# Optimization experiments

Measured on AMD Instinct MI355X. Metric: run time of the kernel, lower is better.

The kernel has to match this reference:

```python
import jax, jax.numpy as jnp
import numpy as np

B, S, D, H = 4, 2048, 768, 12
DH = D // H          # 64 head dim
DF = 4 * D           # 3072 FFN hidden
EPS = 1e-5


def setup_inputs() -> dict:
    key = jax.random.key(0)
    ks = jax.random.split(key, 16)
    s = 0.02
    inp = {
        "Q": jax.random.normal(ks[0], (B, S, D), jnp.float32),
        "K": jax.random.normal(ks[1], (B, S, D), jnp.float32),
        "V": jax.random.normal(ks[2], (B, S, D), jnp.float32),
        "Wq": s * jax.random.normal(ks[3], (D, D), jnp.float32),
        "bq": jnp.zeros((D,), jnp.float32),
        "Wk": s * jax.random.normal(ks[4], (D, D), jnp.float32),
        "bk": jnp.zeros((D,), jnp.float32),
        "Wv": s * jax.random.normal(ks[5], (D, D), jnp.float32),
        "bv": jnp.zeros((D,), jnp.float32),
        "Wo": s * jax.random.normal(ks[6], (D, D), jnp.float32),
        "bo": jnp.zeros((D,), jnp.float32),
        "ln_g": jnp.ones((D,), jnp.float32),
        "ln_b": jnp.zeros((D,), jnp.float32),
        "W1": s * jax.random.normal(ks[7], (D, DF), jnp.float32),
        "b1": jnp.zeros((DF,), jnp.float32),
        "W2": s * jax.random.normal(ks[8], (DF, D), jnp.float32),
        "b2": jnp.zeros((D,), jnp.float32),
    }
    return inp


def _split_heads(x):  # [B,S,D] -> [B,H,S,DH]
    return x.reshape(B, S, H, DH).transpose(0, 2, 1, 3)


def _layernorm(x, g, b):
    mu = jnp.mean(x, axis=-1, keepdims=True)
    var = jnp.mean(jnp.square(x - mu), axis=-1, keepdims=True)
    return (x - mu) * jax.lax.rsqrt(var + EPS) * g + b


def reference(Q, K, V, Wq, bq, Wk, bk, Wv, bv, Wo, bo, ln_g, ln_b, W1, b1, W2, b2):
    q = _split_heads(Q @ Wq + bq)            # [B,H,S,DH]
    k = _split_heads(K @ Wk + bk)
    v = _split_heads(V @ Wv + bv)
    scale = 1.0 / jnp.sqrt(jnp.asarray(DH, q.dtype))
    scores = jnp.einsum("bhqd,bhkd->bhqk", q, k) * scale   # [B,H,S,S]
    attn = jax.nn.softmax(scores, axis=-1)
    ctx = jnp.einsum("bhqk,bhkd->bhqd", attn, v)            # [B,H,S,DH]
    ctx = ctx.transpose(0, 2, 1, 3).reshape(B, S, D)
    attn_out = ctx @ Wo + bo
    h = _layernorm(Q + attn_out, ln_g, ln_b)                # residual + LN
    ff = jax.nn.gelu(h @ W1 + b1, approximate=False) @ W2 + b2
    return ff
```

## Files before the change

### kernel.cpp

```cpp
#include <hip/hip_runtime.h>
#include <hip/hip_bf16.h>
#include <math.h>

#define Bsz 4
#define Ssz 2048
#define Dsz 768
#define Hn  12
#define DHn 64
#define DFn 3072
#define NTOK (Bsz*Ssz)
#define EPSL 1e-5f

typedef __attribute__((ext_vector_type(8))) short bf16x8;
typedef __attribute__((ext_vector_type(4))) float f32x4;

__device__ __forceinline__ unsigned short f2bf(float f) {
    unsigned int u = __float_as_uint(f);
    u += 0x7fffu + ((u >> 16) & 1u);
    return (unsigned short)(u >> 16);
}
__device__ __forceinline__ float bf2f(unsigned short h) {
    return __uint_as_float(((unsigned int)h) << 16);
}

#define GLDS(gp, lp) __builtin_amdgcn_global_load_lds( \
    (const __attribute__((address_space(1))) void*)(gp), \
    (__attribute__((address_space(3))) void*)(lp), 16, 0, 0)

__device__ __forceinline__ void swizzle_mn(int bid, int mtot, int nb, int& m, int& n)
{
    const int xcd = bid & 7;
    const int idx = bid >> 3;
    m = xcd * (mtot >> 3) + idx / nb;
    n = idx % nb;
}

__global__ __launch_bounds__(256)
void wsplit_k(const float* __restrict__ W, unsigned short* __restrict__ Wh,
              unsigned short* __restrict__ Wl, int K, int N)
{
    __shared__ float tile[32][33];
    const int n0 = blockIdx.x * 32, k0 = blockIdx.y * 32;
    const int x = threadIdx.x, y = threadIdx.y;
    #pragma unroll
    for (int i = 0; i < 4; i++)
        tile[y + 8 * i][x] = W[(size_t)(k0 + y + 8 * i) * N + n0 + x];
    __syncthreads();
    #pragma unroll
    for (int i = 0; i < 4; i++) {
        float v = tile[x][y + 8 * i];
        unsigned short hb = f2bf(v);
        size_t o = (size_t)(n0 + y + 8 * i) * K + k0 + x;
        Wh[o] = hb;
        Wl[o] = f2bf(v - bf2f(hb));
    }
}

__global__ __launch_bounds__(256)
void presplit_k(const float* __restrict__ Qf, const float* __restrict__ Kf,
                const float* __restrict__ Vf,
                unsigned short* __restrict__ Qh, unsigned short* __restrict__ Ql,
                unsigned short* __restrict__ Kh, unsigned short* __restrict__ Kl,
                unsigned short* __restrict__ Vh)
{
    const int blocksPerSeg = (NTOK * Dsz) / 2048;
    const int seg = blockIdx.x / blocksPerSeg;
    const int idx = ((blockIdx.x % blocksPerSeg) * 256 + threadIdx.x) * 8;
    const float* src = (seg == 0) ? Qf : (seg == 1) ? Kf : Vf;

    float4 a = *(const float4*)(src + idx);
    float4 b = *(const float4*)(src + idx + 4);
    float fv[8] = {a.x, a.y, a.z, a.w, b.x, b.y, b.z, b.w};

    bf16x8 h8, l8;
    #pragma unroll
    for (int e = 0; e < 8; e++) {
        unsigned short hb = f2bf(fv[e]);
        h8[e] = (short)hb;
        l8[e] = (short)f2bf(fv[e] - bf2f(hb));
    }
    unsigned short* Hp = (seg == 0) ? Qh : (seg == 1) ? Kh : Vh;
    *(bf16x8*)(Hp + idx) = h8;
    if (seg < 2) {
        unsigned short* Lp = (seg == 0) ? Ql : Kl;
        *(bf16x8*)(Lp + idx) = l8;
    }
}

__global__ __launch_bounds__(256)
void qkv_mfma(const unsigned short* __restrict__ Qsh, const unsigned short* __restrict__ Qsl,
              const unsigned short* __restrict__ Ksh, const unsigned short* __restrict__ Ksl,
              const unsigned short* __restrict__ Vsh,
              const unsigned short* __restrict__ Wqh, const unsigned short* __restrict__ Wql,
              const unsigned short* __restrict__ Wkh, const unsigned short* __restrict__ Wkl,
              const unsigned short* __restrict__ Wvh, const unsigned short* __restrict__ Wvl,
              const float* __restrict__ bq, const float* __restrict__ bk,
              const float* __restrict__ bv,
              unsigned short* __restrict__ qh, unsigned short* __restrict__ ql,
              unsigned short* __restrict__ kh, unsigned short* __restrict__ kl,
              unsigned short* __restrict__ vout)
{
    __shared__ short smem[32768];

    const int t    = threadIdx.x;
    const int lane = t & 63;
    const int w    = t >> 6;
    const int wm   = w >> 1;
    const int wn   = w & 1;

    int m_tile, nblk;
    swizzle_mn(blockIdx.x, 192, 6, m_tile, nblk);
    const int which = m_tile / 64;
    const int m0    = (m_tile % 64) * 128;
    const int n0    = nblk * 128;

    const unsigned short* Ah = (which == 0) ? Qsh : (which == 1) ? Ksh : Vsh;
    const unsigned short* Al = (which == 0) ? Qsl : Ksl;
    const unsigned short* Bh = (which == 0) ? Wqh : (which == 1) ? Wkh : Wvh;
    const unsigned short* Bl = (which == 0) ? Wql : (which == 1) ? Wkl : Wvl;
    const float* bias = (which == 0) ? bq : (which == 1) ? bk : bv;

    f32x4 acc[4][4];
    #pragma unroll
    for (int i = 0; i < 4; i++)
        #pragma unroll
        for (int j = 0; j < 4; j++)
            acc[i][j] = (f32x4){0.f, 0.f, 0.f, 0.f};

    const int fr = lane & 15;
    const int q8 = (lane >> 4) * 8;

    auto stage = [&](int buf, int k0) {
        short* base = smem + buf * 16384;
        #pragma unroll
        for (int it = 0; it < 2; it++) {
            const int p   = t + 256 * it;
            const int row = p >> 2;
            const int c8  = (p & 3) * 8;
            GLDS(Ah + (size_t)(m0 + row) * Dsz + k0 + c8, base + p * 8);
            GLDS(Bh + (size_t)(n0 + row) * Dsz + k0 + c8, base + 8192 + p * 8);
            if (which < 2) {
                GLDS(Al + (size_t)(m0 + row) * Dsz + k0 + c8, base + 4096 + p * 8);
                GLDS(Bl + (size_t)(n0 + row) * Dsz + k0 + c8, base + 12288 + p * 8);
            }
        }
    };

    stage(0, 0);
    __syncthreads();
    int cur = 0;
    for (int k0 = 0; k0 < Dsz; k0 += 32) {
        if (k0 + 32 < Dsz) stage(cur ^ 1, k0 + 32);

        short* base = smem + cur * 16384;
        short* As_h = base;
        short* As_l = base + 4096;
        short* Bs_h = base + 8192;
        short* Bs_l = base + 12288;

        bf16x8 a_h[4], a_l[4], b_h[4], b_l[4];
        #pragma unroll
        for (int i = 0; i < 4; i++) {
            const int ra = (wm * 64 + i * 16 + fr) * 32 + q8;
            const int rb = (wn * 64 + i * 16 + fr) * 32 + q8;
            a_h[i] = *(const bf16x8*)&As_h[ra];
            b_h[i] = *(const bf16x8*)&Bs_h[rb];
            if (which < 2) {
                a_l[i] = *(const bf16x8*)&As_l[ra];
                b_l[i] = *(const bf16x8*)&Bs_l[rb];
            }
        }
        if (which < 2) {
            #pragma unroll
            for (int i = 0; i < 4; i++)
                #pragma unroll
                for (int j = 0; j < 4; j++) {
                    acc[i][j] = __builtin_amdgcn_mfma_f32_16x16x32_bf16(a_l[i], b_h[j], acc[i][j], 0, 0, 0);
                    acc[i][j] = __builtin_amdgcn_mfma_f32_16x16x32_bf16(a_h[i], b_l[j], acc[i][j], 0, 0, 0);
                    acc[i][j] = __builtin_amdgcn_mfma_f32_16x16x32_bf16(a_h[i], b_h[j], acc[i][j], 0, 0, 0);
                }
        } else {
            #pragma unroll
            for (int i = 0; i < 4; i++)
                #pragma unroll
                for (int j = 0; j < 4; j++)
                    acc[i][j] = __builtin_amdgcn_mfma_f32_16x16x32_bf16(a_h[i], b_h[j], acc[i][j], 0, 0, 0);
        }
        __syncthreads();
        cur ^= 1;
    }

    const int quad = lane >> 4;
    #pragma unroll
    for (int i = 0; i < 4; i++)
        #pragma unroll
        for (int j = 0; j < 4; j++) {
            const int n  = n0 + wn * 64 + j * 16 + fr;
            const float bn = bias[n];
            const int hh = n >> 6, dh = n & 63;
            #pragma unroll
            for (int r = 0; r < 4; r++) {
                const int m = m0 + wm * 64 + i * 16 + quad * 4 + r;
                const int bb = m >> 11, s = m & 2047;
                const size_t o = (((size_t)bb * Hn + hh) * Ssz + s) * DHn + dh;
                float v = acc[i][j][r] + bn;
                if (which == 0) {
                    v *= 0.125f;
                    unsigned short hb = f2bf(v);
                    qh[o] = hb; ql[o] = f2bf(v - bf2f(hb));
                } else if (which == 1) {
                    unsigned short hb = f2bf(v);
                    kh[o] = hb; kl[o] = f2bf(v - bf2f(hb));
                } else {
                    vout[o] = f2bf(v);
                }
            }
        }
}

__global__ __launch_bounds__(256)
void vtrans_k(const unsigned short* __restrict__ src, unsigned short* __restrict__ dst)
{
    __shared__ unsigned short tl[32][33];
    const int s0 = blockIdx.x * 32;
    const int d0 = blockIdx.y * 32;
    const int hd = blockIdx.z;
    const int x = threadIdx.x, y = threadIdx.y;
    const size_t base = (size_t)hd * Ssz * DHn;
    #pragma unroll
    for (int i = 0; i < 4; i++)
        tl[y + 8 * i][x] = src[base + (size_t)(s0 + y + 8 * i) * DHn + d0 + x];
    __syncthreads();
    #pragma unroll
    for (int i = 0; i < 4; i++)
        dst[base + (size_t)(d0 + y + 8 * i) * Ssz + s0 + x] = tl[x][y + 8 * i];
}

template<int MODE, bool ASPLIT, bool BSPLIT, int BM>
__global__ __launch_bounds__(256)
void gemm_mfma(const unsigned short* __restrict__ Ah, const unsigned short* __restrict__ Al,
               const unsigned short* __restrict__ Bh, const unsigned short* __restrict__ Bl,
               const float* __restrict__ bias, const float* __restrict__ res,
               float* __restrict__ Cf, unsigned short* __restrict__ Cb,
               int M, int N, int K)
{
    constexpr int MI = BM / 32;
    constexpr int AE = BM * 32;
    constexpr int NA = ASPLIT ? 2 : 1;
    constexpr int NB = BSPLIT ? 2 : 1;
    constexpr int BUFE = AE * NA + 4096 * NB;
    __shared__ short smem[2 * BUFE];

    const int t    = threadIdx.x;
    const int lane = t & 63;
    const int w    = t >> 6;
    const int wm   = w >> 1;
    const int wn   = w & 1;

    int mt, nt_;
    swizzle_mn(blockIdx.x, M / BM, N >> 7, mt, nt_);
    const int m0 = mt * BM;
    const int n0 = nt_ * 128;

    f32x4 acc[MI][4];
    #pragma unroll
    for (int i = 0; i < MI; i++)
        #pragma unroll
        for (int j = 0; j < 4; j++)
            acc[i][j] = (f32x4){0.f, 0.f, 0.f, 0.f};

    const int fr = lane & 15;
    const int q8 = (lane >> 4) * 8;

    auto stage = [&](int buf, int k0) {
        short* base = smem + buf * BUFE;
        #pragma unroll
        for (int it = 0; it < BM / 64; it++) {
            const int p   = t + 256 * it;
            const int row = p >> 2;
            const int c8  = (p & 3) * 8;
            GLDS(Ah + (size_t)(m0 + row) * K + k0 + c8, base + p * 8);
            if (ASPLIT)
                GLDS(Al + (size_t)(m0 + row) * K + k0 + c8, base + AE + p * 8);
        }
        short* bbase = base + AE * NA;
        #pragma unroll
        for (int it = 0; it < 2; it++) {
            const int p   = t + 256 * it;
            const int row = p >> 2;
            const int c8  = (p & 3) * 8;
            GLDS(Bh + (size_t)(n0 + row) * K + k0 + c8, bbase + p * 8);
            if (BSPLIT)
                GLDS(Bl + (size_t)(n0 + row) * K + k0 + c8, bbase + 4096 + p * 8);
        }
    };

    stage(0, 0);
    __syncthreads();
    int cur = 0;
    for (int k0 = 0; k0 < K; k0 += 32) {
        if (k0 + 32 < K) stage(cur ^ 1, k0 + 32);

        short* base = smem + cur * BUFE;
        short* As_h = base;
        short* As_l = base + AE;
        short* Bs_h = base + AE * NA;
        short* Bs_l = Bs_h + 4096;

        bf16x8 a_h[MI], a_l[MI], b_h[4], b_l[4];
        #pragma unroll
        for (int i = 0; i < MI; i++) {
            const int ra = (wm * (BM / 2) + i * 16 + fr) * 32 + q8;
            a_h[i] = *(const bf16x8*)&As_h[ra];
            if (ASPLIT) a_l[i] = *(const bf16x8*)&As_l[ra];
        }
        #pragma unroll
        for (int j = 0; j < 4; j++) {
            const int rb = (wn * 64 + j * 16 + fr) * 32 + q8;
            b_h[j] = *(const bf16x8*)&Bs_h[rb];
            if (BSPLIT) b_l[j] = *(const bf16x8*)&Bs_l[rb];
        }
        #pragma unroll
        for (int i = 0; i < MI; i++)
            #pragma unroll
            for (int j = 0; j < 4; j++) {
                if (ASPLIT)
                    acc[i][j] = __builtin_amdgcn_mfma_f32_16x16x32_bf16(a_l[i], b_h[j], acc[i][j], 0, 0, 0);
                if (BSPLIT)
                    acc[i][j] = __builtin_amdgcn_mfma_f32_16x16x32_bf16(a_h[i], b_l[j], acc[i][j], 0, 0, 0);
                acc[i][j] = __builtin_amdgcn_mfma_f32_16x16x32_bf16(a_h[i], b_h[j], acc[i][j], 0, 0, 0);
            }
        __syncthreads();
        cur ^= 1;
    }

    const int quad = lane >> 4;
    #pragma unroll
    for (int i = 0; i < MI; i++)
        #pragma unroll
        for (int j = 0; j < 4; j++) {
            const int n  = n0 + wn * 64 + j * 16 + fr;
            const float bn = bias[n];
            #pragma unroll
            for (int r = 0; r < 4; r++) {
                const int m = m0 + wm * (BM / 2) + i * 16 + quad * 4 + r;
                float v = acc[i][j][r] + bn;
                if (MODE == 1) {
                    v += res[(size_t)m * N + n];
                    Cf[(size_t)m * N + n] = v;
                } else if (MODE == 2) {
                    v = 0.5f * v * (1.0f + erff(v * 0.70710678118654752f));
                    Cb[(size_t)m * N + n] = f2bf(v);
                } else {
                    Cf[(size_t)m * N + n] = v;
                }
            }
        }
}

__device__ __forceinline__ void stage16(const unsigned short* src, short* dst,
                                        int p0, int lane, int row0, int rstride, int col0)
{
    const int p   = p0 + lane;
    const int n   = p >> 3;
    const int cst = (p & 7) ^ (n & 7);
    const unsigned short* g = src + (size_t)(row0 + n) * rstride + col0 + cst * 8;
    GLDS(g, dst + p0 * 8);
}

__device__ __forceinline__ bf16x8 frag(const short* arr, int row, int c)
{
    const int pos = row * 8 + (c ^ (row & 7));
    return *(const bf16x8*)&arr[pos * 8];
}

__global__ __launch_bounds__(256)
void attn_mfma(const unsigned short* __restrict__ qh, const unsigned short* __restrict__ ql,
               const unsigned short* __restrict__ kh, const unsigned short* __restrict__ kl,
               const unsigned short* __restrict__ vt, unsigned short* __restrict__ ch)
{
    const int hid = blockIdx.x;
    const int b   = hid / Hn;
    const int h   = hid - b * Hn;
    const int q0  = blockIdx.y * 64;
    const int t    = threadIdx.x;
    const int lane = t & 63;
    const int w    = t >> 6;
    const int fr   = lane & 15;
    const int quad = lane >> 4;

    __shared__ short sKV[12288];
    __shared__ short sQP[8192];
    short* Kh_s = sKV;
    short* Kl_s = sKV + 4096;
    short* Vh_s = sKV + 8192;
    short* Qh_s = sQP;
    short* Ql_s = sQP + 4096;
    float* Pw   = (float*)sQP + w * 1024;

    const size_t hoff = (size_t)hid * Ssz * DHn;

    stage16(qh + hoff, Qh_s, w * 128,      lane, q0, DHn, 0);
    stage16(qh + hoff, Qh_s, w * 128 + 64, lane, q0, DHn, 0);
    stage16(ql + hoff, Ql_s, w * 128,      lane, q0, DHn, 0);
    stage16(ql + hoff, Ql_s, w * 128 + 64, lane, q0, DHn, 0);

    f32x4 O[4];
    #pragma unroll
    for (int d = 0; d < 4; d++) O[d] = (f32x4){0.f, 0.f, 0.f, 0.f};
    float lp[4] = {0.f, 0.f, 0.f, 0.f};

    bf16x8 qfh[2], qfl[2];

    for (int kt = 0; kt < Ssz / 64; kt++) {
        __syncthreads();
        const int kr = kt * 64;
        #pragma unroll
        for (int bt = 0; bt < 2; bt++) {
            const int p0 = w * 128 + bt * 64;
            stage16(kh + hoff, Kh_s, p0, lane, kr, DHn, 0);
            stage16(kl + hoff, Kl_s, p0, lane, kr, DHn, 0);
            stage16(vt + hoff, Vh_s, p0, lane, 0, Ssz, kr);
        }
        __syncthreads();

        if (kt == 0) {
            #pragma unroll
            for (int kc = 0; kc < 2; kc++) {
                qfh[kc] = frag(Qh_s, w * 16 + fr, kc * 4 + quad);
                qfl[kc] = frag(Ql_s, w * 16 + fr, kc * 4 + quad);
            }
            __syncthreads();
        }

        f32x4 sc[4];
        #pragma unroll
        for (int nt = 0; nt < 4; nt++) sc[nt] = (f32x4){0.f, 0.f, 0.f, 0.f};
        __builtin_amdgcn_s_setprio(1);
        #pragma unroll
        for (int nt = 0; nt < 4; nt++)
            #pragma unroll
            for (int kc = 0; kc < 2; kc++) {
                bf16x8 bh = frag(Kh_s, nt * 16 + fr, kc * 4 + quad);
                bf16x8 bl = frag(Kl_s, nt * 16 + fr, kc * 4 + quad);
                sc[nt] = __builtin_amdgcn_mfma_f32_16x16x32_bf16(qfl[kc], bh, sc[nt], 0, 0, 0);
                sc[nt] = __builtin_amdgcn_mfma_f32_16x16x32_bf16(qfh[kc], bl, sc[nt], 0, 0, 0);
                sc[nt] = __builtin_amdgcn_mfma_f32_16x16x32_bf16(qfh[kc], bh, sc[nt], 0, 0, 0);
            }
        __builtin_amdgcn_s_setprio(0);

        #pragma unroll
        for (int r = 0; r < 4; r++) {
            const int m = quad * 4 + r;
            #pragma unroll
            for (int nt = 0; nt < 4; nt++) {
                float p = __expf(sc[nt][r]);
                const int j  = nt * 16 + fr;
                const int c4 = j >> 2;
                Pw[(m * 16 + (c4 ^ m)) * 4 + (j & 3)] = p;
                lp[r] += p;
            }
        }

        #pragma unroll
        for (int kc = 0; kc < 2; kc++) {
            const int c4a = kc * 8 + quad * 2;
            float4 pa = *(float4*)&Pw[(fr * 16 + (c4a ^ fr)) * 4];
            float4 pb = *(float4*)&Pw[(fr * 16 + ((c4a + 1) ^ fr)) * 4];
            union { bf16x8 v; __hip_bfloat162 b2[4]; } P;
            P.b2[0] = __float22bfloat162_rn(make_float2(pa.x, pa.y));
            P.b2[1] = __float22bfloat162_rn(make_float2(pa.z, pa.w));
            P.b2[2] = __float22bfloat162_rn(make_float2(pb.x, pb.y));
            P.b2[3] = __float22bfloat162_rn(make_float2(pb.z, pb.w));
            __builtin_amdgcn_s_setprio(1);
            #pragma unroll
            for (int dt = 0; dt < 4; dt++) {
                bf16x8 vh = frag(Vh_s, dt * 16 + fr, kc * 4 + quad);
                O[dt] = __builtin_amdgcn_mfma_f32_16x16x32_bf16(P.v, vh, O[dt], 0, 0, 0);
            }
            __builtin_amdgcn_s_setprio(0);
        }
    }

    #pragma unroll
    for (int r = 0; r < 4; r++) {
        float ls = lp[r];
        #pragma unroll
        for (int msk = 1; msk < 16; msk <<= 1) ls += __shfl_xor(ls, msk);
        const float linv = 1.0f / ls;
        const int s = q0 + w * 16 + quad * 4 + r;
        unsigned short* och = ch + ((size_t)b * Ssz + s) * Dsz + h * DHn;
        #pragma unroll
        for (int dt = 0; dt < 4; dt++)
            och[dt * 16 + fr] = f2bf(O[dt][r] * linv);
    }
}

__global__ __launch_bounds__(256)
void ln_k(const float* __restrict__ x, const float* __restrict__ g,
          const float* __restrict__ bb, unsigned short* __restrict__ yh)
{
    const int row = blockIdx.x;
    const float* xr = x + (size_t)row * Dsz;
    unsigned short* yhr = yh + (size_t)row * Dsz;
    const int t = threadIdx.x;

    float v0 = xr[t], v1 = xr[t + 256], v2 = xr[t + 512];
    float s = v0 + v1 + v2;
    #pragma unroll
    for (int o = 1; o < 64; o <<= 1) s += __shfl_xor(s, o, 64);

    __shared__ float red1[4];
    __shared__ float red2[4];
    const int wid = t >> 6, lane = t & 63;
    if (lane == 0) red1[wid] = s;
    __syncthreads();
    const float mean = (red1[0] + red1[1] + red1[2] + red1[3]) * (1.0f / Dsz);

    float d0 = v0 - mean, d1 = v1 - mean, d2 = v2 - mean;
    float vs = d0 * d0 + d1 * d1 + d2 * d2;
    #pragma unroll
    for (int o = 1; o < 64; o <<= 1) vs += __shfl_xor(vs, o, 64);
    if (lane == 0) red2[wid] = vs;
    __syncthreads();
    const float var = (red2[0] + red2[1] + red2[2] + red2[3]) * (1.0f / Dsz);
    const float inv = rsqrtf(var + EPSL);

    yhr[t]       = f2bf(d0 * inv * g[t]       + bb[t]);
    yhr[t + 256] = f2bf(d1 * inv * g[t + 256] + bb[t + 256]);
    yhr[t + 512] = f2bf(d2 * inv * g[t + 512] + bb[t + 512]);
}

extern "C" void kernel_launch(void* const* d_in, const int* in_sizes, int n_in,
                              void* d_out, int out_size, void* d_ws, size_t ws_size,
                              hipStream_t stream)
{
    (void)in_sizes; (void)n_in; (void)out_size; (void)ws_size;
    const float* Q    = (const float*)d_in[0];
    const float* Kin  = (const float*)d_in[1];
    const float* Vin  = (const float*)d_in[2];
    const float* Wq   = (const float*)d_in[3];
    const float* bq   = (const float*)d_in[4];
    const float* Wk   = (const float*)d_in[5];
    const float* bk   = (const float*)d_in[6];
    const float* Wv   = (const float*)d_in[7];
    const float* bv   = (const float*)d_in[8];
    const float* Wo   = (const float*)d_in[9];
    const float* bo   = (const float*)d_in[10];
    const float* ln_g = (const float*)d_in[11];
    const float* ln_b = (const float*)d_in[12];
    const float* W1   = (const float*)d_in[13];
    const float* b1   = (const float*)d_in[14];
    const float* W2   = (const float*)d_in[15];
    const float* b2   = (const float*)d_in[16];
    float* out = (float*)d_out;

    const size_t NT = (size_t)NTOK * Dsz;
    unsigned short* usws = (unsigned short*)d_ws;
    unsigned short* qh  = usws + 0 * NT;
    unsigned short* ql  = usws + 1 * NT;
    unsigned short* kh  = usws + 2 * NT;
    unsigned short* kl  = usws + 3 * NT;
    unsigned short* vt  = usws + 4 * NT;
    unsigned short* ch  = usws + 6 * NT;
    unsigned short* wsp = usws + 8 * NT;
    const size_t SW = (size_t)Dsz * Dsz;
    unsigned short* Wqh = wsp + 0 * SW;
    unsigned short* Wql = wsp + 1 * SW;
    unsigned short* Wkh = wsp + 2 * SW;
    unsigned short* Wkl = wsp + 3 * SW;
    unsigned short* Wvh = wsp + 4 * SW;
    unsigned short* Wvl = wsp + 5 * SW;
    unsigned short* Woh = wsp + 6 * SW;
    unsigned short* Wol = wsp + 7 * SW;
    unsigned short* W1h = wsp + 8 * SW;
    unsigned short* W1l = wsp + 12 * SW;
    unsigned short* W2h = wsp + 16 * SW;
    unsigned short* W2l = wsp + 20 * SW;
    float*          hpre = (float*)usws;
    unsigned short* hh   = kh;
    unsigned short* hbuf = usws + 4 * NT;

    unsigned short* Qsh = usws + 4 * NT;
    unsigned short* Qsl = usws + 5 * NT;
    unsigned short* Ksh = usws + 7 * NT;
    unsigned short* Ksl = (unsigned short*)d_out;
    unsigned short* Vsh = (unsigned short*)d_out + NT;

    dim3 wb(32, 8);
    wsplit_k<<<dim3(Dsz / 32, Dsz / 32), wb, 0, stream>>>(Wq, Wqh, Wql, Dsz, Dsz);
    wsplit_k<<<dim3(Dsz / 32, Dsz / 32), wb, 0, stream>>>(Wk, Wkh, Wkl, Dsz, Dsz);
    wsplit_k<<<dim3(Dsz / 32, Dsz / 32), wb, 0, stream>>>(Wv, Wvh, Wvl, Dsz, Dsz);
    wsplit_k<<<dim3(Dsz / 32, Dsz / 32), wb, 0, stream>>>(Wo, Woh, Wol, Dsz, Dsz);
    wsplit_k<<<dim3(DFn / 32, Dsz / 32), wb, 0, stream>>>(W1, W1h, W1l, Dsz, DFn);
    wsplit_k<<<dim3(Dsz / 32, DFn / 32), wb, 0, stream>>>(W2, W2h, W2l, DFn, Dsz);

    presplit_k<<<3 * (NTOK * Dsz / 2048), 256, 0, stream>>>(
        Q, Kin, Vin, Qsh, Qsl, Ksh, Ksl, Vsh);

    qkv_mfma<<<1152, 256, 0, stream>>>(
        Qsh, Qsl, Ksh, Ksl, Vsh,
        Wqh, Wql, Wkh, Wkl, Wvh, Wvl, bq, bk, bv,
        qh, ql, kh, kl, ch);

    vtrans_k<<<dim3(Ssz / 32, DHn / 32, Bsz * Hn), wb, 0, stream>>>(ch, vt);

    attn_mfma<<<dim3(Bsz * Hn, Ssz / 64), 256, 0, stream>>>(qh, ql, kh, kl, vt, ch);

    gemm_mfma<1, false, true, 64><<<768, 256, 0, stream>>>(
        ch, nullptr, Woh, Wol, bo, Q, hpre, nullptr, NTOK, Dsz, Dsz);

    ln_k<<<NTOK, 256, 0, stream>>>(hpre, ln_g, ln_b, hh);

    gemm_mfma<2, false, true, 128><<<1536, 256, 0, stream>>>(
        hh, nullptr, W1h, W1l, b1, nullptr, nullptr, hbuf, NTOK, DFn, Dsz);
    gemm_mfma<3, false, false, 64><<<768, 256, 0, stream>>>(
        hbuf, nullptr, W2h, nullptr, b2, nullptr, out, nullptr, NTOK, Dsz, DFn);
}
```

Before: 602.4 us.

## Double-buffer K/V tiles in attention kernel to overlap loads with MFMA

Allocates two shared-memory buffers for the K/V tiles and loads the next tile before computing on the current one. One barrier per iteration replaces the two used before. Q fragments are loaded once before the loop, and the P scratch gets its own buffer. This targets global-load latency stalls, at the cost of more LDS per block and possibly lower occupancy.

```diff
diff --git a/kernel.cpp b/kernel.cpp
--- a/kernel.cpp
+++ b/kernel.cpp
@@ -389,49 +389,52 @@
     const int fr   = lane & 15;
     const int quad = lane >> 4;
 
-    __shared__ short sKV[12288];
-    __shared__ short sQP[8192];
-    short* Kh_s = sKV;
-    short* Kl_s = sKV + 4096;
-    short* Vh_s = sKV + 8192;
-    short* Qh_s = sQP;
-    short* Ql_s = sQP + 4096;
-    float* Pw   = (float*)sQP + w * 1024;
+    __shared__ short sKV[24576];
+    __shared__ float Pws[4096];
+    float* Pw = Pws + w * 1024;
 
     const size_t hoff = (size_t)hid * Ssz * DHn;
 
-    stage16(qh + hoff, Qh_s, w * 128,      lane, q0, DHn, 0);
-    stage16(qh + hoff, Qh_s, w * 128 + 64, lane, q0, DHn, 0);
-    stage16(ql + hoff, Ql_s, w * 128,      lane, q0, DHn, 0);
-    stage16(ql + hoff, Ql_s, w * 128 + 64, lane, q0, DHn, 0);
+    stage16(qh + hoff, sKV,        w * 128,      lane, q0, DHn, 0);
+    stage16(qh + hoff, sKV,        w * 128 + 64, lane, q0, DHn, 0);
+    stage16(ql + hoff, sKV + 4096, w * 128,      lane, q0, DHn, 0);
+    stage16(ql + hoff, sKV + 4096, w * 128 + 64, lane, q0, DHn, 0);
+    __syncthreads();
+    bf16x8 qfh[2], qfl[2];
+    #pragma unroll
+    for (int kc = 0; kc < 2; kc++) {
+        qfh[kc] = frag(sKV,        w * 16 + fr, kc * 4 + quad);
+        qfl[kc] = frag(sKV + 4096, w * 16 + fr, kc * 4 + quad);
+    }
+    __syncthreads();
+
+    auto stageKV = [&](int buf, int kt) {
+        short* base = sKV + buf * 12288;
+        const int kr = kt * 64;
+        #pragma unroll
+        for (int bt = 0; bt < 2; bt++) {
+            const int p0 = w * 128 + bt * 64;
+            stage16(kh + hoff, base,        p0, lane, kr, DHn, 0);
+            stage16(kl + hoff, base + 4096, p0, lane, kr, DHn, 0);
+            stage16(vt + hoff, base + 8192, p0, lane, 0, Ssz, kr);
+        }
+    };
 
     f32x4 O[4];
     #pragma unroll
     for (int d = 0; d < 4; d++) O[d] = (f32x4){0.f, 0.f, 0.f, 0.f};
     float lp[4] = {0.f, 0.f, 0.f, 0.f};
 
-    bf16x8 qfh[2], qfl[2];
-
+    stageKV(0, 0);
+    __syncthreads();
+    int cur = 0;
     for (int kt = 0; kt < Ssz / 64; kt++) {
-        __syncthreads();
-        const int kr = kt * 64;
-        #pragma unroll
-        for (int bt = 0; bt < 2; bt++) {
-            const int p0 = w * 128 + bt * 64;
-            stage16(kh + hoff, Kh_s, p0, lane, kr, DHn, 0);
-            stage16(kl + hoff, Kl_s, p0, lane, kr, DHn, 0);
-            stage16(vt + hoff, Vh_s, p0, lane, 0, Ssz, kr);
-        }
-        __syncthreads();
-
-        if (kt == 0) {
-            #pragma unroll
-            for (int kc = 0; kc < 2; kc++) {
-                qfh[kc] = frag(Qh_s, w * 16 + fr, kc * 4 + quad);
-                qfl[kc] = frag(Ql_s, w * 16 + fr, kc * 4 + quad);
-            }
-            __syncthreads();
-        }
+        if (kt + 1 < Ssz / 64) stageKV(cur ^ 1, kt + 1);
+
+        short* base = sKV + cur * 12288;
+        short* Kh_s = base;
+        short* Kl_s = base + 4096;
+        short* Vh_s = base + 8192;
 
         f32x4 sc[4];
         #pragma unroll
@@ -480,6 +483,8 @@
             }
             __builtin_amdgcn_s_setprio(0);
         }
+        __syncthreads();
+        cur ^= 1;
     }
 
     #pragma unroll
```

New measurement: 628.0 us. +4.2%, slower.
